# Kernel tuning notes

Measured on AMD Instinct MI355X. Metric: run time of the kernel, lower is better.

Reference implementation:

```python
import jax, jax.numpy as jnp
import numpy as np

WH, WW = 7, 7
NUM_HEADS = 8

def _relative_position_index(Wh, Ww):
    coords = np.stack(np.meshgrid(np.arange(Wh), np.arange(Ww), indexing='ij'))  # (2, Wh, Ww)
    cf = coords.reshape(2, -1)                       # (2, N)
    rc = cf[:, :, None] - cf[:, None, :]             # (2, N, N)
    rc = rc.transpose(1, 2, 0).astype(np.int64)      # (N, N, 2)
    rc[..., 0] += Wh - 1
    rc[..., 1] += Ww - 1
    rc[..., 0] *= 2 * Ww - 1
    return rc.sum(-1)                                # (N, N)

_REL_IDX = jnp.asarray(_relative_position_index(WH, WW))


def setup_inputs() -> dict:
    key = jax.random.key(0)
    ks = jax.random.split(key, 9)
    B_, N, C = 2048, 49, 256
    nW = 64
    return {
        'x': jax.random.normal(ks[0], (B_, N, C), jnp.float32),
        'mask': jax.random.normal(ks[1], (nW, N, N), jnp.float32),
        'sal_fg_attn_mask': jax.random.normal(ks[2], (B_, N, N), jnp.float32),
        'sal_bg_attn_mask': jax.random.normal(ks[3], (B_, N, N), jnp.float32),
        'qkv_w': jax.random.normal(ks[4], (3 * C, C), jnp.float32) * 0.02,
        'qkv_b': jax.random.normal(ks[5], (3 * C,), jnp.float32) * 0.02,
        'proj_w': jax.random.normal(ks[6], (C, C), jnp.float32) * 0.02,
        'proj_b': jax.random.normal(ks[7], (C,), jnp.float32) * 0.02,
        'rel_pos_bias_table': jax.random.normal(ks[8], ((2 * WH - 1) * (2 * WW - 1), NUM_HEADS), jnp.float32) * 0.02,
    }


def reference(x, mask, sal_fg_attn_mask, sal_bg_attn_mask, qkv_w, qkv_b, proj_w, proj_b, rel_pos_bias_table):
    B_, N, C = x.shape
    H = NUM_HEADS
    hd = C // H
    scale = hd ** -0.5

    qkv = x @ qkv_w.T + qkv_b                        # (B_, N, 3C)
    qkv = qkv.reshape(B_, N, 3, H, hd).transpose(2, 0, 3, 1, 4)  # (3, B_, H, N, hd)
    q, k, v = qkv[0] * scale, qkv[1], qkv[2]

    attn = jnp.einsum('bhqd,bhkd->bhqk', q, k)       # (B_, H, N, N)
    bias = rel_pos_bias_table[_REL_IDX]              # (N, N, H)
    attn = attn + bias.transpose(2, 0, 1)[None]      # broadcast over B_

    attn_fg = attn + sal_fg_attn_mask[:, None]
    attn_bg = attn + sal_bg_attn_mask[:, None]

    nW = mask.shape[0]
    m = mask[None, :, None]                          # (1, nW, 1, N, N)

    def masked_softmax(a):
        a = a.reshape(B_ // nW, nW, H, N, N) + m
        return jax.nn.softmax(a.reshape(B_, H, N, N), axis=-1)

    attn = masked_softmax(attn)
    attn_fg = masked_softmax(attn_fg)
    attn_bg = masked_softmax(attn_bg)

    def av(a):
        return jnp.einsum('bhqk,bhkd->bqhd', a, v).reshape(B_, N, C)

    out = av(attn) + av(attn_fg) - av(attn_bg)
    return out @ proj_w.T + proj_b
```

## Files before the change

### kernel.cpp

```cpp
#include <hip/hip_runtime.h>
#include <hip/hip_bf16.h>
#include <math.h>


#define B_TOT   2048
#define NTOK    49
#define CDIM    256
#define NHEAD   8
#define HDIM    32
#define MROWS   (B_TOT * NTOK)
#define QKV_N   (3 * CDIM)

typedef __attribute__((ext_vector_type(8))) short short8;
typedef __attribute__((ext_vector_type(4))) float floatx4;

typedef unsigned int u32_g __attribute__((address_space(1)));
typedef unsigned int u32_l __attribute__((address_space(3)));

__device__ __forceinline__ void gld_lds16(const void* g, void* l) {
    __builtin_amdgcn_global_load_lds((const u32_g*)g, (u32_l*)l, 16, 0, 0);
}

__global__ __launch_bounds__(256) void cast_kernel(
    const float* __restrict__ in, __hip_bfloat16* __restrict__ out, int n8)
{
    const int i = blockIdx.x * 256 + threadIdx.x;
    if (i >= n8) return;
    const float4* p = (const float4*)in + (size_t)i * 2;
    float4 a = p[0], b = p[1];
    __hip_bfloat16 r[8];
    r[0] = __float2bfloat16(a.x); r[1] = __float2bfloat16(a.y);
    r[2] = __float2bfloat16(a.z); r[3] = __float2bfloat16(a.w);
    r[4] = __float2bfloat16(b.x); r[5] = __float2bfloat16(b.y);
    r[6] = __float2bfloat16(b.z); r[7] = __float2bfloat16(b.w);
    *(uint4*)(out + (size_t)i * 8) = *(const uint4*)r;
}

template<int NDIM, bool OUT_BF16>
__global__ __launch_bounds__(256) void gemm_mfma(
    const __hip_bfloat16* __restrict__ A,
    const __hip_bfloat16* __restrict__ W,
    const float* __restrict__ bias,
    void* __restrict__ Yv)
{
    const int K = 256;
    __shared__ short As[128 * 64];
    __shared__ short Bs[128 * 64];
    const int t = threadIdx.x;
    const int lane = t & 63, w = t >> 6;
    const int wr = w >> 1, wc = w & 1;
    const int q = lane >> 4, l15 = lane & 15;
    const int m0 = blockIdx.y * 128, n0 = blockIdx.x * 128;

    const int srow = t >> 3, skb = t & 7;
    const int gkb = skb ^ (srow & 7);
    const __hip_bfloat16* Ag = A + (size_t)(m0 + srow) * K + gkb * 8;
    const __hip_bfloat16* Wg = W + (size_t)(n0 + srow) * K + gkb * 8;

    floatx4 acc[4][4] = {};
    const int swz = l15 & 7;

    for (int k0 = 0; k0 < K; k0 += 64) {
        __syncthreads();
        #pragma unroll
        for (int i = 0; i < 4; i++) {
            gld_lds16(Ag + (size_t)(i * 32) * K + k0, &As[i * 2048 + w * 512]);
            gld_lds16(Wg + (size_t)(i * 32) * K + k0, &Bs[i * 2048 + w * 512]);
        }
        __syncthreads();
        #pragma unroll
        for (int kk = 0; kk < 2; kk++) {
            const int kbs = ((kk << 2) + q) ^ swz;
            short8 af[4], bf[4];
            #pragma unroll
            for (int i = 0; i < 4; i++) {
                af[i] = *(const short8*)&As[(wr * 64 + i * 16 + l15) * 64 + kbs * 8];
                bf[i] = *(const short8*)&Bs[(wc * 64 + i * 16 + l15) * 64 + kbs * 8];
            }
            #pragma unroll
            for (int i = 0; i < 4; i++)
                #pragma unroll
                for (int j = 0; j < 4; j++)
                    acc[i][j] = __builtin_amdgcn_mfma_f32_16x16x32_bf16(
                        af[i], bf[j], acc[i][j], 0, 0, 0);
        }
    }

    #pragma unroll
    for (int j = 0; j < 4; j++) {
        const int n = n0 + wc * 64 + j * 16 + l15;
        const float bv = bias[n];
        #pragma unroll
        for (int i = 0; i < 4; i++) {
            #pragma unroll
            for (int r = 0; r < 4; r++) {
                const int m = m0 + wr * 64 + i * 16 + q * 4 + r;
                const float val = acc[i][j][r] + bv;
                if (OUT_BF16)
                    ((__hip_bfloat16*)Yv)[(size_t)m * NDIM + n] = __float2bfloat16(val);
                else
                    ((float*)Yv)[(size_t)m * NDIM + n] = val;
            }
        }
    }
}

__global__ __launch_bounds__(256, 4) void attn_kernel(
    const __hip_bfloat16* __restrict__ Y,
    const float* __restrict__ wmask,
    const float* __restrict__ fg,
    const float* __restrict__ bg,
    const float* __restrict__ table,
    __hip_bfloat16* __restrict__ O)
{
    __shared__ __hip_bfloat16 sQ[64 * 40];
    __shared__ __hip_bfloat16 sK[64 * 40];
    __shared__ __hip_bfloat16 sVt[32 * 72];
    __shared__ __hip_bfloat16 sP[64 * 72];
    __shared__ float stab[169];

    const int blk = blockIdx.x;
    const int b = blk >> 3, h = blk & 7;
    const int t = threadIdx.x;
    const int w = t >> 6, lane = t & 63;
    const int quad = lane >> 4, l15 = lane & 15;
    const float scale = 0.17677669529663687f;

    const float* wm  = wmask + (size_t)(b & 63) * (NTOK * NTOK);
    const float* fgb = fg + (size_t)b * (NTOK * NTOK);
    const float* bgb = bg + (size_t)b * (NTOK * NTOK);
    float mwm[16], mfg[16], mbg[16];
    #pragma unroll
    for (int r = 0; r < 4; r++) {
        const int row = w * 16 + quad * 4 + r;
        #pragma unroll
        for (int nt = 0; nt < 4; nt++) {
            const int col = nt * 16 + l15;
            const int sidx = (row < NTOK && col < NTOK) ? row * NTOK + col : 0;
            mwm[r * 4 + nt] = wm[sidx];
            mfg[r * 4 + nt] = fgb[sidx];
            mbg[r * 4 + nt] = bgb[sidx];
        }
    }
    if (t < 169) stab[t] = table[t * 8 + h];
    const __hip_bfloat16* Yb = Y + (size_t)b * NTOK * QKV_N + h * HDIM;
    if (t < 196) {
        const int n = t >> 2, c = t & 3;
        uint4 qv = *(const uint4*)(Yb + (size_t)n * QKV_N + c * 8);
        uint4 kv = *(const uint4*)(Yb + (size_t)n * QKV_N + 256 + c * 8);
        uint4 vv = *(const uint4*)(Yb + (size_t)n * QKV_N + 512 + c * 8);
        *(uint4*)(sQ + n * 40 + c * 8) = qv;
        *(uint4*)(sK + n * 40 + c * 8) = kv;
        const __hip_bfloat16* vp = (const __hip_bfloat16*)&vv;
        #pragma unroll
        for (int j = 0; j < 8; j++)
            sVt[(c * 8 + j) * 72 + n] = vp[j];
    }
    {
        const __hip_bfloat16 z = __float2bfloat16(0.f);
        #pragma unroll
        for (int it = 0; it < 2; it++) {
            const int idx = t + it * 256;
            const int d = idx >> 4, c = 49 + (idx & 15);
            sVt[d * 72 + c] = z;
        }
    }
    __syncthreads();

    floatx4 acc[4];
    {
        short8 af = *(const short8*)(sQ + (w * 16 + l15) * 40 + quad * 8);
        #pragma unroll
        for (int nt = 0; nt < 4; nt++) {
            short8 bf = *(const short8*)(sK + (nt * 16 + l15) * 40 + quad * 8);
            floatx4 z = {};
            acc[nt] = __builtin_amdgcn_mfma_f32_16x16x32_bf16(af, bf, z, 0, 0, 0);
        }
    }

    float xbase[16];
    #pragma unroll
    for (int r = 0; r < 4; r++) {
        const int row = w * 16 + quad * 4 + r;
        const int rc = min(row, 48);
        const int qi = (rc * 146) >> 10, qj = rc - qi * 7;
        #pragma unroll
        for (int nt = 0; nt < 4; nt++) {
            const int col = nt * 16 + l15;
            const int cc = min(col, 48);
            const int ki = (cc * 146) >> 10, kj = cc - ki * 7;
            const float tb = stab[(qi - ki + 6) * 13 + (qj - kj + 6)];
            const float s = acc[nt][r] * scale + tb + mwm[r * 4 + nt];
            xbase[r * 4 + nt] = (col < NTOK) ? s : -1e30f;
        }
    }

    float pc[16];
    #pragma unroll
    for (int i = 0; i < 16; i++) pc[i] = 0.f;
    #pragma unroll
    for (int v = 0; v < 3; v++) {
        float xv[16];
        #pragma unroll
        for (int i = 0; i < 16; i++)
            xv[i] = (v == 0) ? xbase[i] + mfg[i]
                  : (v == 1) ? xbase[i] + mbg[i]
                  : xbase[i];
        float mr[4];
        #pragma unroll
        for (int r = 0; r < 4; r++)
            mr[r] = fmaxf(fmaxf(xv[r * 4], xv[r * 4 + 1]),
                          fmaxf(xv[r * 4 + 2], xv[r * 4 + 3]));
        #pragma unroll
        for (int st = 1; st < 16; st <<= 1)
            #pragma unroll
            for (int r = 0; r < 4; r++)
                mr[r] = fmaxf(mr[r], __shfl_xor(mr[r], st));
        #pragma unroll
        for (int i = 0; i < 16; i++)
            xv[i] = __expf(xv[i] - mr[i >> 2]);
        float sr[4];
        #pragma unroll
        for (int r = 0; r < 4; r++)
            sr[r] = (xv[r * 4] + xv[r * 4 + 1]) + (xv[r * 4 + 2] + xv[r * 4 + 3]);
        #pragma unroll
        for (int st = 1; st < 16; st <<= 1)
            #pragma unroll
            for (int r = 0; r < 4; r++)
                sr[r] += __shfl_xor(sr[r], st);
        #pragma unroll
        for (int r = 0; r < 4; r++)
            sr[r] = __builtin_amdgcn_rcpf(sr[r]);
        const float sgn = (v == 1) ? -1.f : 1.f;
        #pragma unroll
        for (int i = 0; i < 16; i++)
            pc[i] += sgn * xv[i] * sr[i >> 2];
    }

    #pragma unroll
    for (int r = 0; r < 4; r++) {
        const int row = w * 16 + quad * 4 + r;
        #pragma unroll
        for (int nt = 0; nt < 4; nt++)
            sP[row * 72 + nt * 16 + l15] = __float2bfloat16(pc[r * 4 + nt]);
    }
    __syncthreads();

    floatx4 o0 = {}, o1 = {};
    {
        short8 a0  = *(const short8*)(sP + (w * 16 + l15) * 72 + quad * 8);
        short8 a1  = *(const short8*)(sP + (w * 16 + l15) * 72 + 32 + quad * 8);
        short8 b00 = *(const short8*)(sVt + l15 * 72 + quad * 8);
        short8 b01 = *(const short8*)(sVt + l15 * 72 + 32 + quad * 8);
        short8 b10 = *(const short8*)(sVt + (16 + l15) * 72 + quad * 8);
        short8 b11 = *(const short8*)(sVt + (16 + l15) * 72 + 32 + quad * 8);
        o0 = __builtin_amdgcn_mfma_f32_16x16x32_bf16(a0, b00, o0, 0, 0, 0);
        o0 = __builtin_amdgcn_mfma_f32_16x16x32_bf16(a1, b01, o0, 0, 0, 0);
        o1 = __builtin_amdgcn_mfma_f32_16x16x32_bf16(a0, b10, o1, 0, 0, 0);
        o1 = __builtin_amdgcn_mfma_f32_16x16x32_bf16(a1, b11, o1, 0, 0, 0);
    }
    __hip_bfloat16* Ob = O + (size_t)b * NTOK * CDIM + h * HDIM;
    #pragma unroll
    for (int r = 0; r < 4; r++) {
        const int m = w * 16 + quad * 4 + r;
        if (m < NTOK) {
            Ob[(size_t)m * CDIM + l15]      = __float2bfloat16(o0[r]);
            Ob[(size_t)m * CDIM + 16 + l15] = __float2bfloat16(o1[r]);
        }
    }
}

extern "C" void kernel_launch(void* const* d_in, const int* in_sizes, int n_in,
                              void* d_out, int out_size, void* d_ws, size_t ws_size,
                              hipStream_t stream) {
    const float* x      = (const float*)d_in[0];
    const float* mask   = (const float*)d_in[1];
    const float* fg     = (const float*)d_in[2];
    const float* bg     = (const float*)d_in[3];
    const float* qkv_w  = (const float*)d_in[4];
    const float* qkv_b  = (const float*)d_in[5];
    const float* proj_w = (const float*)d_in[6];
    const float* proj_b = (const float*)d_in[7];
    const float* table  = (const float*)d_in[8];
    float* out = (float*)d_out;

    char* ws = (char*)d_ws;
    __hip_bfloat16* xb  = (__hip_bfloat16*)(ws);
    __hip_bfloat16* Ybf = (__hip_bfloat16*)(ws + 51380224);
    __hip_bfloat16* Obf = (__hip_bfloat16*)(ws + 205520896);
    __hip_bfloat16* qwb = (__hip_bfloat16*)(ws + 256901120);
    __hip_bfloat16* pwb = (__hip_bfloat16*)(ws + 257294336);

    dim3 blk(256);
    cast_kernel<<<dim3((MROWS * CDIM / 8 + 255) / 256), blk, 0, stream>>>(x, xb, MROWS * CDIM / 8);
    cast_kernel<<<dim3((QKV_N * CDIM / 8 + 255) / 256), blk, 0, stream>>>(qkv_w, qwb, QKV_N * CDIM / 8);
    cast_kernel<<<dim3((CDIM * CDIM / 8 + 255) / 256), blk, 0, stream>>>(proj_w, pwb, CDIM * CDIM / 8);

    gemm_mfma<QKV_N, true><<<dim3(QKV_N / 128, MROWS / 128), blk, 0, stream>>>(xb, qwb, qkv_b, Ybf);
    attn_kernel<<<dim3(B_TOT * NHEAD), blk, 0, stream>>>(Ybf, mask, fg, bg, table, Obf);
    gemm_mfma<CDIM, false><<<dim3(CDIM / 128, MROWS / 128), blk, 0, stream>>>(Obf, pwb, proj_b, out);
}
```

Baseline: 438.2 us.

## Factor softmax exponentials via precomputed exp masks and fused bias tables

After: 396.4 us. 9.6% less time.

```diff
diff --git a/kernel.cpp b/kernel.cpp
--- a/kernel.cpp
+++ b/kernel.cpp
@@ -10,6 +10,14 @@
 #define HDIM    32
 #define MROWS   (B_TOT * NTOK)
 #define QKV_N   (3 * CDIM)
+
+#define LOG2E 1.4426950408889634f
+
+#if __has_builtin(__builtin_amdgcn_exp2f)
+#define EXP2(x) __builtin_amdgcn_exp2f(x)
+#else
+#define EXP2(x) __expf((x) * 0.6931471805599453f)
+#endif
 
 typedef __attribute__((ext_vector_type(8))) short short8;
 typedef __attribute__((ext_vector_type(4))) float floatx4;
@@ -36,6 +44,35 @@
     *(uint4*)(out + (size_t)i * 8) = *(const uint4*)r;
 }
 
+__global__ __launch_bounds__(256) void prep_wmask(
+    const float* __restrict__ wmask,
+    const float* __restrict__ table,
+    float* __restrict__ wmp)
+{
+    const int idx = blockIdx.x * 256 + threadIdx.x;
+    const int col = idx & 63, row = (idx >> 6) & 63;
+    const int h = (idx >> 12) & 7, win = idx >> 15;
+    float v = -1e30f;
+    if (row < 49 && col < 49) {
+        const int qi = row / 7, qj = row % 7;
+        const int ki = col / 7, kj = col % 7;
+        const int ti = (qi - ki + 6) * 13 + (qj - kj + 6);
+        v = (wmask[win * 2401 + row * 49 + col] + table[ti * 8 + h]) * LOG2E;
+    }
+    wmp[idx] = v;
+}
+
+__global__ __launch_bounds__(256) void prep_expmask(
+    const float* __restrict__ in, float* __restrict__ out)
+{
+    const int i = blockIdx.x * 256 + threadIdx.x;
+    float4 a = ((const float4*)in)[i];
+    float4 r;
+    r.x = EXP2(a.x * LOG2E); r.y = EXP2(a.y * LOG2E);
+    r.z = EXP2(a.z * LOG2E); r.w = EXP2(a.w * LOG2E);
+    ((float4*)out)[i] = r;
+}
+
 template<int NDIM, bool OUT_BF16>
 __global__ __launch_bounds__(256) void gemm_mfma(
     const __hip_bfloat16* __restrict__ A,
@@ -50,7 +87,12 @@
     const int lane = t & 63, w = t >> 6;
     const int wr = w >> 1, wc = w & 1;
     const int q = lane >> 4, l15 = lane & 15;
-    const int m0 = blockIdx.y * 128, n0 = blockIdx.x * 128;
+
+    constexpr int NBX = NDIM / 128;
+    constexpr int NWG = NBX * (MROWS / 128);
+    int bid = blockIdx.y * NBX + blockIdx.x;
+    bid = (bid & 7) * (NWG >> 3) + (bid >> 3);
+    const int m0 = (bid / NBX) * 128, n0 = (bid % NBX) * 128;
 
     const int srow = t >> 3, skb = t & 7;
     const int gkb = skb ^ (srow & 7);
@@ -107,42 +149,42 @@
 
 __global__ __launch_bounds__(256, 4) void attn_kernel(
     const __hip_bfloat16* __restrict__ Y,
-    const float* __restrict__ wmask,
-    const float* __restrict__ fg,
-    const float* __restrict__ bg,
-    const float* __restrict__ table,
+    const float* __restrict__ wmp,
+    const float* __restrict__ Fgp,
+    const float* __restrict__ Bgp,
     __hip_bfloat16* __restrict__ O)
 {
     __shared__ __hip_bfloat16 sQ[64 * 40];
     __shared__ __hip_bfloat16 sK[64 * 40];
     __shared__ __hip_bfloat16 sVt[32 * 72];
     __shared__ __hip_bfloat16 sP[64 * 72];
-    __shared__ float stab[169];
 
     const int blk = blockIdx.x;
-    const int b = blk >> 3, h = blk & 7;
+    const int b = (blk >> 6) * 8 + (blk & 7);
+    const int h = (blk >> 3) & 7;
     const int t = threadIdx.x;
     const int w = t >> 6, lane = t & 63;
     const int quad = lane >> 4, l15 = lane & 15;
-    const float scale = 0.17677669529663687f;
-
-    const float* wm  = wmask + (size_t)(b & 63) * (NTOK * NTOK);
-    const float* fgb = fg + (size_t)b * (NTOK * NTOK);
-    const float* bgb = bg + (size_t)b * (NTOK * NTOK);
+    const float SC = 0.17677669529663687f * LOG2E;
+
+    const float* wmb = wmp + (((size_t)(b & 63) * 8 + h) << 12);
+    const float* fgb = Fgp + (size_t)b * (NTOK * NTOK);
+    const float* bgb = Bgp + (size_t)b * (NTOK * NTOK);
     float mwm[16], mfg[16], mbg[16];
     #pragma unroll
     for (int r = 0; r < 4; r++) {
         const int row = w * 16 + quad * 4 + r;
-        #pragma unroll
-        for (int nt = 0; nt < 4; nt++) {
-            const int col = nt * 16 + l15;
-            const int sidx = (row < NTOK && col < NTOK) ? row * NTOK + col : 0;
-            mwm[r * 4 + nt] = wm[sidx];
-            mfg[r * 4 + nt] = fgb[sidx];
-            mbg[r * 4 + nt] = bgb[sidx];
-        }
-    }
-    if (t < 169) stab[t] = table[t * 8 + h];
+        const int rc49 = min(row, 48) * 49;
+        const float* pw = wmb + row * 64 + l15;
+        const float* pf = fgb + rc49 + l15;
+        const float* pb = bgb + rc49 + l15;
+        mwm[r * 4 + 0] = pw[0];  mwm[r * 4 + 1] = pw[16];
+        mwm[r * 4 + 2] = pw[32]; mwm[r * 4 + 3] = pw[48];
+        mfg[r * 4 + 0] = pf[0];  mfg[r * 4 + 1] = pf[16];
+        mfg[r * 4 + 2] = pf[32]; mfg[r * 4 + 3] = fgb[rc49 + 48];
+        mbg[r * 4 + 0] = pb[0];  mbg[r * 4 + 1] = pb[16];
+        mbg[r * 4 + 2] = pb[32]; mbg[r * 4 + 3] = bgb[rc49 + 48];
+    }
     const __hip_bfloat16* Yb = Y + (size_t)b * NTOK * QKV_N + h * HDIM;
     if (t < 196) {
         const int n = t >> 2, c = t & 3;
@@ -157,6 +199,11 @@
             sVt[(c * 8 + j) * 72 + n] = vp[j];
     }
     {
+        unsigned int* pK = (unsigned int*)sK;
+        #pragma unroll
+        for (int i = 980 + t; i < 1280; i += 256) pK[i] = 0u;
+    }
+    {
         const __hip_bfloat16 z = __float2bfloat16(0.f);
         #pragma unroll
         for (int it = 0; it < 2; it++) {
@@ -178,63 +225,44 @@
         }
     }
 
-    float xbase[16];
-    #pragma unroll
-    for (int r = 0; r < 4; r++) {
-        const int row = w * 16 + quad * 4 + r;
-        const int rc = min(row, 48);
-        const int qi = (rc * 146) >> 10, qj = rc - qi * 7;
+    float e0[16];
+    #pragma unroll
+    for (int r = 0; r < 4; r++)
+        #pragma unroll
+        for (int nt = 0; nt < 4; nt++)
+            e0[r * 4 + nt] = EXP2(fmaf(acc[nt][r], SC, mwm[r * 4 + nt]));
+    #pragma unroll
+    for (int i = 0; i < 16; i++) mfg[i] *= e0[i];
+    #pragma unroll
+    for (int i = 0; i < 16; i++) mbg[i] *= e0[i];
+
+    float s0[4], sf[4], sb[4];
+    #pragma unroll
+    for (int r = 0; r < 4; r++) {
+        s0[r] = (e0[r * 4] + e0[r * 4 + 1]) + (e0[r * 4 + 2] + e0[r * 4 + 3]);
+        sf[r] = (mfg[r * 4] + mfg[r * 4 + 1]) + (mfg[r * 4 + 2] + mfg[r * 4 + 3]);
+        sb[r] = (mbg[r * 4] + mbg[r * 4 + 1]) + (mbg[r * 4 + 2] + mbg[r * 4 + 3]);
+    }
+    #pragma unroll
+    for (int st = 1; st < 16; st <<= 1)
+        #pragma unroll
+        for (int r = 0; r < 4; r++) {
+            s0[r] += __shfl_xor(s0[r], st);
+            sf[r] += __shfl_xor(sf[r], st);
+            sb[r] += __shfl_xor(sb[r], st);
+        }
+
+    float pc[16];
+    #pragma unroll
+    for (int r = 0; r < 4; r++) {
+        const float r0 = __builtin_amdgcn_rcpf(s0[r]);
+        const float rf = __builtin_amdgcn_rcpf(sf[r]);
+        const float rb = -__builtin_amdgcn_rcpf(sb[r]);
         #pragma unroll
         for (int nt = 0; nt < 4; nt++) {
-            const int col = nt * 16 + l15;
-            const int cc = min(col, 48);
-            const int ki = (cc * 146) >> 10, kj = cc - ki * 7;
-            const float tb = stab[(qi - ki + 6) * 13 + (qj - kj + 6)];
-            const float s = acc[nt][r] * scale + tb + mwm[r * 4 + nt];
-            xbase[r * 4 + nt] = (col < NTOK) ? s : -1e30f;
-        }
-    }
-
-    float pc[16];
-    #pragma unroll
-    for (int i = 0; i < 16; i++) pc[i] = 0.f;
-    #pragma unroll
-    for (int v = 0; v < 3; v++) {
-        float xv[16];
-        #pragma unroll
-        for (int i = 0; i < 16; i++)
-            xv[i] = (v == 0) ? xbase[i] + mfg[i]
-                  : (v == 1) ? xbase[i] + mbg[i]
-                  : xbase[i];
-        float mr[4];
-        #pragma unroll
-        for (int r = 0; r < 4; r++)
-            mr[r] = fmaxf(fmaxf(xv[r * 4], xv[r * 4 + 1]),
-                          fmaxf(xv[r * 4 + 2], xv[r * 4 + 3]));
-        #pragma unroll
-        for (int st = 1; st < 16; st <<= 1)
-            #pragma unroll
-            for (int r = 0; r < 4; r++)
-                mr[r] = fmaxf(mr[r], __shfl_xor(mr[r], st));
-        #pragma unroll
-        for (int i = 0; i < 16; i++)
-            xv[i] = __expf(xv[i] - mr[i >> 2]);
-        float sr[4];
-        #pragma unroll
-        for (int r = 0; r < 4; r++)
-            sr[r] = (xv[r * 4] + xv[r * 4 + 1]) + (xv[r * 4 + 2] + xv[r * 4 + 3]);
-        #pragma unroll
-        for (int st = 1; st < 16; st <<= 1)
-            #pragma unroll
-            for (int r = 0; r < 4; r++)
-                sr[r] += __shfl_xor(sr[r], st);
-        #pragma unroll
-        for (int r = 0; r < 4; r++)
-            sr[r] = __builtin_amdgcn_rcpf(sr[r]);
-        const float sgn = (v == 1) ? -1.f : 1.f;
-        #pragma unroll
-        for (int i = 0; i < 16; i++)
-            pc[i] += sgn * xv[i] * sr[i >> 2];
+            const int i = r * 4 + nt;
+            pc[i] = fmaf(mbg[i], rb, fmaf(mfg[i], rf, e0[i] * r0));
+        }
     }
 
     #pragma unroll
@@ -290,6 +318,9 @@
     __hip_bfloat16* Obf = (__hip_bfloat16*)(ws + 205520896);
     __hip_bfloat16* qwb = (__hip_bfloat16*)(ws + 256901120);
     __hip_bfloat16* pwb = (__hip_bfloat16*)(ws + 257294336);
+    float* wmp = (float*)(ws);
+    float* Fgp = (float*)(ws + 8388608);
+    float* Bgp = (float*)(ws + 28057600);
 
     dim3 blk(256);
     cast_kernel<<<dim3((MROWS * CDIM / 8 + 255) / 256), blk, 0, stream>>>(x, xb, MROWS * CDIM / 8);
@@ -297,6 +328,11 @@
     cast_kernel<<<dim3((CDIM * CDIM / 8 + 255) / 256), blk, 0, stream>>>(proj_w, pwb, CDIM * CDIM / 8);
 
     gemm_mfma<QKV_N, true><<<dim3(QKV_N / 128, MROWS / 128), blk, 0, stream>>>(xb, qwb, qkv_b, Ybf);
-    attn_kernel<<<dim3(B_TOT * NHEAD), blk, 0, stream>>>(Ybf, mask, fg, bg, table, Obf);
+
+    prep_wmask<<<dim3(8192), blk, 0, stream>>>(mask, table, wmp);
+    prep_expmask<<<dim3(4802), blk, 0, stream>>>(fg, Fgp);
+    prep_expmask<<<dim3(4802), blk, 0, stream>>>(bg, Bgp);
+
+    attn_kernel<<<dim3(B_TOT * NHEAD), blk, 0, stream>>>(Ybf, wmp, Fgp, Bgp, Obf);
     gemm_mfma<CDIM, false><<<dim3(CDIM / 128, MROWS / 128), blk, 0, stream>>>(Obf, pwb, proj_b, out);
 }
```
